# Optimization experiments

Hardware: AMD Instinct MI355X
Metric: run time of the kernel (lower is better)

Reference implementation:

```python
import jax, jax.numpy as jnp
import numpy as np

NEG = jnp.float32(-1e9)


def setup_inputs() -> dict:
    key = jax.random.key(0)
    ks = jax.random.split(key, 8)
    B, S, D = 8, 2048, 1024
    scale = 1.0 / np.sqrt(D)
    return {
        "xQ": jax.random.normal(ks[0], (B, S, D), jnp.float32),
        "xK": jax.random.normal(ks[1], (B, S, D), jnp.float32),
        "xV": jax.random.normal(ks[2], (B, S, D), jnp.float32),
        "padding_mask": jax.random.randint(ks[3], (B, S), 0, 2, jnp.int32),
        "casual_mask": jnp.ones((B, S), jnp.int32),
        "W_q": jax.random.normal(ks[4], (D, D), jnp.float32) * scale,
        "b_q": jnp.zeros((D,), jnp.float32),
        "W_k": jax.random.normal(ks[5], (D, D), jnp.float32) * scale,
        "b_k": jnp.zeros((D,), jnp.float32),
        "W_v": jax.random.normal(ks[6], (D, D), jnp.float32) * scale,
        "b_v": jnp.zeros((D,), jnp.float32),
    }


def reference(xQ, xK, xV, padding_mask, casual_mask, W_q, b_q, W_k, b_k, W_v, b_v):
    # Linear projections (torch nn.Linear: x @ W.T + b)
    Q = jnp.einsum('bsd,ed->bse', xQ, W_q) + b_q
    K = jnp.einsum('bsd,ed->bse', xK, W_k) + b_k
    V = jnp.einsum('bsd,ed->bse', xV, W_v) + b_v

    # Raw logits (note: original code applies NO 1/sqrt(dk) scaling)
    QKT = jnp.einsum('bqd,bkd->bqk', Q, K)  # [B, Sq, Sk]

    # Additive padding mask: -1e9 on padded key positions
    pad = jnp.where(padding_mask[:, None, :] == 0, NEG, jnp.float32(0.0))
    # Additive causal mask: -1e9 above the diagonal
    Sq, Sk = QKT.shape[1], QKT.shape[2]
    caus = jnp.where(
        jnp.tril(jnp.ones((Sq, Sk), dtype=bool)), jnp.float32(0.0), NEG
    )[None, :, :]
    QKT = QKT + pad + caus

    S = jax.nn.softmax(QKT, axis=-1)
    return jnp.einsum('bqk,bkd->bqd', S, V)
```

## Files before the change

kernel.cpp:

```cpp
#include <hip/hip_runtime.h>

typedef __attribute__((ext_vector_type(4))) float f4;
typedef __attribute__((ext_vector_type(4))) float f32x4;
typedef _Float16 half8 __attribute__((ext_vector_type(8)));

#define DEVI static __device__ __forceinline__

DEVI void gload_lds16(const void* g, void* l) {
  __builtin_amdgcn_global_load_lds(
      (const __attribute__((address_space(1))) void*)g,
      (__attribute__((address_space(3))) void*)l, 16, 0, 0);
}

DEVI int xcd_swz(int id, int n) {
  int q = n >> 3, r = n & 7;
  int x = id & 7, c = id >> 3;
  return (x < r ? x * (q + 1) : r * (q + 1) + (x - r) * q) + c;
}

#define FENCED_BARRIER()                \
  __builtin_amdgcn_sched_barrier(0);    \
  __builtin_amdgcn_s_barrier();         \
  __builtin_amdgcn_sched_barrier(0);

#define SWZ(kgv, rowv) ((((kgv) ^ ((rowv) >> 1)) & 3) * 8)

__global__ __launch_bounds__(256) void cvt_plain(const float* __restrict__ X,
                                                 _Float16* __restrict__ H,
                                                 int n4) {
  int i = blockIdx.x * 256 + threadIdx.x;
  const int stride = gridDim.x * 256;
  typedef _Float16 half4v __attribute__((ext_vector_type(4)));
  for (; i < n4; i += stride) {
    f4 x = ((const f4*)X)[i];
    half4v h;
#pragma unroll
    for (int j = 0; j < 4; ++j) h[j] = (_Float16)x[j];
    ((half4v*)H)[i] = h;
  }
}

__global__ __launch_bounds__(256) void cvt_split(const float* __restrict__ X,
                                                 _Float16* __restrict__ H,
                                                 _Float16* __restrict__ L,
                                                 int n4) {
  int i = blockIdx.x * 256 + threadIdx.x;
  const int stride = gridDim.x * 256;
  typedef _Float16 half4v __attribute__((ext_vector_type(4)));
  for (; i < n4; i += stride) {
    f4 x = ((const f4*)X)[i];
    half4v h, l;
#pragma unroll
    for (int j = 0; j < 4; ++j) {
      h[j] = (_Float16)x[j];
      l[j] = (_Float16)(x[j] - (float)h[j]);
    }
    ((half4v*)H)[i] = h;
    ((half4v*)L)[i] = l;
  }
}

DEVI void acc_zero44(f32x4 (&acc)[4][4]) {
#pragma unroll
  for (int i = 0; i < 4; ++i)
#pragma unroll
    for (int j = 0; j < 4; ++j) acc[i][j] = (f32x4)0.0f;
}
DEVI void acc_zero42(f32x4 (&acc)[4][2]) {
#pragma unroll
  for (int i = 0; i < 4; ++i)
#pragma unroll
    for (int j = 0; j < 2; ++j) acc[i][j] = (f32x4)0.0f;
}

template <int WSPLIT, int OUTMODE>
__global__ __launch_bounds__(512, 4) void proj3(
    const _Float16* __restrict__ X, const _Float16* __restrict__ Wh,
    const _Float16* __restrict__ Wl, const float* __restrict__ bias,
    _Float16* __restrict__ OutHi, _Float16* __restrict__ OutLo,
    _Float16* __restrict__ VtOut) {
  extern __shared__ _Float16 lds[];
  constexpr int ACH = 128 * 32;
  constexpr int BCH = 128 * 32;
  constexpr int CHUNK = ACH + BCH * (1 + WSPLIT);
  const int id = xcd_swz(blockIdx.x, gridDim.x);
  const int m0 = (id >> 3) * 128, n0 = (id & 7) * 128;
  const _Float16* A0 = X + (size_t)m0 * 1024;
  const _Float16* B0 = Wh + (size_t)n0 * 1024;
  const _Float16* B1 = Wl + (size_t)n0 * 1024;
  const int tid = threadIdx.x;
  const int w = tid >> 6, lane = tid & 63;
  const int wm = w >> 2, wn = w & 3;
  const int r16 = lane & 15, kg = lane >> 4;
  f32x4 acc[4][2];
  acc_zero42(acc);

  auto STAGE = [&](int t, int buf) {
    _Float16* base = lds + buf * CHUNK;
    int row = tid >> 2, c = tid & 3;
    int cs = (c ^ (row >> 1)) & 3;
    size_t src = (size_t)row * 1024 + t * 32 + cs * 8;
    gload_lds16(A0 + src, base + tid * 8);
    gload_lds16(B0 + src, base + ACH + tid * 8);
    if (WSPLIT) gload_lds16(B1 + src, base + ACH + BCH + tid * 8);
  };
  auto COMPUTE = [&](int buf) {
    const _Float16* la = lds + buf * CHUNK;
    const _Float16* lb = la + ACH;
    half8 a[4], b0f[2], b1f[2];
#pragma unroll
    for (int mi = 0; mi < 4; ++mi) {
      int row = wm * 64 + mi * 16 + r16;
      a[mi] = *(const half8*)(la + row * 32 + SWZ(kg, row));
    }
#pragma unroll
    for (int ni = 0; ni < 2; ++ni) {
      int row = wn * 32 + ni * 16 + r16;
      int off = row * 32 + SWZ(kg, row);
      b0f[ni] = *(const half8*)(lb + off);
      if (WSPLIT) b1f[ni] = *(const half8*)(lb + BCH + off);
    }
    __builtin_amdgcn_s_setprio(1);
#pragma unroll
    for (int mi = 0; mi < 4; ++mi)
#pragma unroll
      for (int ni = 0; ni < 2; ++ni) {
        acc[mi][ni] = __builtin_amdgcn_mfma_f32_16x16x32_f16(
            a[mi], b0f[ni], acc[mi][ni], 0, 0, 0);
        if (WSPLIT)
          acc[mi][ni] = __builtin_amdgcn_mfma_f32_16x16x32_f16(
              a[mi], b1f[ni], acc[mi][ni], 0, 0, 0);
      }
    __builtin_amdgcn_s_setprio(0);
  };

  const int NS = 32;
  STAGE(0, 0);
  STAGE(1, 1);
  int tt = 0;
  for (; tt < NS - 1; ++tt) {
    if constexpr (WSPLIT)
      asm volatile("s_waitcnt vmcnt(3)" ::: "memory");
    else
      asm volatile("s_waitcnt vmcnt(2)" ::: "memory");
    FENCED_BARRIER();
    if (tt + 2 < NS) STAGE(tt + 2, (tt + 2) % 3);
    COMPUTE(tt % 3);
  }
  asm volatile("s_waitcnt vmcnt(0)" ::: "memory");
  FENCED_BARRIER();
  COMPUTE(tt % 3);

  float bcol[2];
#pragma unroll
  for (int ni = 0; ni < 2; ++ni) bcol[ni] = bias[n0 + wn * 32 + ni * 16 + r16];

  if (OUTMODE != 2) {
#pragma unroll
    for (int mi = 0; mi < 4; ++mi) {
      int row = m0 + wm * 64 + mi * 16 + kg * 4;
#pragma unroll
      for (int ni = 0; ni < 2; ++ni) {
        int col = n0 + wn * 32 + ni * 16 + r16;
#pragma unroll
        for (int j = 0; j < 4; ++j) {
          float v = acc[mi][ni][j] + bcol[ni];
          _Float16 h = (_Float16)v;
          OutHi[(size_t)(row + j) * 1024 + col] = h;
          if (OUTMODE == 0)
            OutLo[(size_t)(row + j) * 1024 + col] = (_Float16)(v - (float)h);
        }
      }
    }
  } else {
    __syncthreads();
    _Float16(*T)[128] = (_Float16(*)[128])lds;
#pragma unroll
    for (int mi = 0; mi < 4; ++mi) {
      int ml = wm * 64 + mi * 16 + kg * 4;
#pragma unroll
      for (int ni = 0; ni < 2; ++ni) {
        int nl = wn * 32 + ni * 16 + r16;
#pragma unroll
        for (int j = 0; j < 4; ++j)
          T[nl][ml + j] = (_Float16)(acc[mi][ni][j] + bcol[ni]);
      }
    }
    __syncthreads();
    const int b = m0 >> 11;
    const int s0 = m0 & 2047;
#pragma unroll
    for (int r = 0; r < 4; ++r) {
      int flat = tid + r * 512;
      int n = flat >> 4, c = flat & 15;
      half8 v = *(const half8*)&T[n][c * 8];
      *(half8*)(VtOut + (size_t)b * (1024 * 2048) + (size_t)(n0 + n) * 2048 +
                s0 + c * 8) = v;
    }
  }
}

template <int WSPLIT, int OUTMODE>
__global__ __launch_bounds__(512, 2) void proj_fused(
    const float* __restrict__ X, const _Float16* __restrict__ Wh,
    const _Float16* __restrict__ Wl, const float* __restrict__ bias,
    _Float16* __restrict__ OutHi, _Float16* __restrict__ OutLo,
    _Float16* __restrict__ VtOut) {
  extern __shared__ _Float16 lds[];
  constexpr int ACH = 256 * 32;
  constexpr int BCH = 128 * 32;
  constexpr int CHUNK = ACH + BCH * (1 + WSPLIT);
  const int id = xcd_swz(blockIdx.x, gridDim.x);
  const int m0 = (id >> 3) * 256, n0 = (id & 7) * 128;
  const float* A = X + (size_t)m0 * 1024;
  const _Float16* B0 = Wh + (size_t)n0 * 1024;
  const _Float16* B1 = Wl + (size_t)n0 * 1024;
  const int tid = threadIdx.x;
  const int w = tid >> 6, lane = tid & 63;
  const int wm = w >> 1, wn = w & 1;
  const int r16 = lane & 15, kg = lane >> 4;
  f32x4 acc[4][4];
  acc_zero44(acc);
  f4 ra[4];

  auto ALOAD = [&](int t) {
#pragma unroll
    for (int j = 0; j < 2; ++j) {
      int g = tid + j * 512;
      int row = g >> 2, c = g & 3;
      const float* src = A + (size_t)row * 1024 + t * 32 + c * 8;
      ra[2 * j] = *(const f4*)src;
      ra[2 * j + 1] = *(const f4*)(src + 4);
    }
  };
  auto AWRITE = [&](int buf) {
    _Float16* ab = lds + buf * CHUNK;
#pragma unroll
    for (int j = 0; j < 2; ++j) {
      int g = tid + j * 512;
      int row = g >> 2, c = g & 3;
      half8 h;
#pragma unroll
      for (int e = 0; e < 4; ++e) {
        h[e] = (_Float16)ra[2 * j][e];
        h[e + 4] = (_Float16)ra[2 * j + 1][e];
      }
      *(half8*)(ab + (size_t)row * 32 + SWZ(c, row)) = h;
    }
  };
  auto WLOAD = [&](int t, int buf) {
    _Float16* bb = lds + buf * CHUNK + ACH;
    int row = tid >> 2, c = tid & 3;
    int cs = (c ^ (row >> 1)) & 3;
    gload_lds16(B0 + (size_t)row * 1024 + t * 32 + cs * 8, bb + tid * 8);
    if (WSPLIT)
      gload_lds16(B1 + (size_t)row * 1024 + t * 32 + cs * 8,
                  bb + BCH + tid * 8);
  };
  auto COMPUTE = [&](int buf) {
    const _Float16* la = lds + buf * CHUNK;
    const _Float16* lb = la + ACH;
    half8 a[4], b0f[4], b1f[4];
#pragma unroll
    for (int mi = 0; mi < 4; ++mi) {
      int row = wm * 64 + mi * 16 + r16;
      a[mi] = *(const half8*)(la + row * 32 + SWZ(kg, row));
    }
#pragma unroll
    for (int ni = 0; ni < 4; ++ni) {
      int row = wn * 64 + ni * 16 + r16;
      int off = row * 32 + SWZ(kg, row);
      b0f[ni] = *(const half8*)(lb + off);
      if (WSPLIT) b1f[ni] = *(const half8*)(lb + BCH + off);
    }
    __builtin_amdgcn_s_setprio(1);
#pragma unroll
    for (int mi = 0; mi < 4; ++mi)
#pragma unroll
      for (int ni = 0; ni < 4; ++ni) {
        acc[mi][ni] = __builtin_amdgcn_mfma_f32_16x16x32_f16(
            a[mi], b0f[ni], acc[mi][ni], 0, 0, 0);
        if (WSPLIT)
          acc[mi][ni] = __builtin_amdgcn_mfma_f32_16x16x32_f16(
              a[mi], b1f[ni], acc[mi][ni], 0, 0, 0);
      }
    __builtin_amdgcn_s_setprio(0);
  };

  const int NS = 32;
  WLOAD(0, 0);
  ALOAD(0);
  asm volatile("s_waitcnt vmcnt(0)" ::: "memory");
  __builtin_amdgcn_sched_barrier(0);
  AWRITE(0);
  asm volatile("s_waitcnt lgkmcnt(0)" ::: "memory");
  FENCED_BARRIER();
  for (int t = 0; t < NS; ++t) {
    if (t + 1 < NS) {
      WLOAD(t + 1, (t + 1) & 1);
      ALOAD(t + 1);
    }
    COMPUTE(t & 1);
    if (t + 1 < NS) {
      asm volatile("s_waitcnt vmcnt(0)" ::: "memory");
      __builtin_amdgcn_sched_barrier(0);
      AWRITE((t + 1) & 1);
      asm volatile("s_waitcnt lgkmcnt(0)" ::: "memory");
      FENCED_BARRIER();
    }
  }

  float bcol[4];
#pragma unroll
  for (int ni = 0; ni < 4; ++ni) bcol[ni] = bias[n0 + wn * 64 + ni * 16 + r16];

  if (OUTMODE != 2) {
#pragma unroll
    for (int mi = 0; mi < 4; ++mi) {
      int row = m0 + wm * 64 + mi * 16 + kg * 4;
#pragma unroll
      for (int ni = 0; ni < 4; ++ni) {
        int col = n0 + wn * 64 + ni * 16 + r16;
#pragma unroll
        for (int j = 0; j < 4; ++j) {
          float v = acc[mi][ni][j] + bcol[ni];
          _Float16 h = (_Float16)v;
          OutHi[(size_t)(row + j) * 1024 + col] = h;
          if (OUTMODE == 0)
            OutLo[(size_t)(row + j) * 1024 + col] = (_Float16)(v - (float)h);
        }
      }
    }
  } else {
    __syncthreads();
    _Float16(*T)[256] = (_Float16(*)[256])lds;
#pragma unroll
    for (int mi = 0; mi < 4; ++mi) {
      int ml = wm * 64 + mi * 16 + kg * 4;
#pragma unroll
      for (int ni = 0; ni < 4; ++ni) {
        int nl = wn * 64 + ni * 16 + r16;
#pragma unroll
        for (int j = 0; j < 4; ++j)
          T[nl][ml + j] = (_Float16)(acc[mi][ni][j] + bcol[ni]);
      }
    }
    __syncthreads();
    const int b = m0 >> 11;
    const int s0 = m0 & 2047;
#pragma unroll
    for (int r = 0; r < 8; ++r) {
      int flat = tid + r * 512;
      int n = flat >> 5, c = flat & 31;
      half8 v = *(const half8*)&T[n][c * 8];
      *(half8*)(VtOut + (size_t)b * (1024 * 2048) + (size_t)(n0 + n) * 2048 +
                s0 + c * 8) = v;
    }
  }
}

__global__ __launch_bounds__(512, 4) void qk_eng(
    const _Float16* __restrict__ Qh, const _Float16* __restrict__ Ql,
    const _Float16* __restrict__ Kh, float* __restrict__ Lg, int bbase) {
  extern __shared__ _Float16 lds[];
  constexpr int CHUNK = 12288;
  const int id = xcd_swz(blockIdx.x, gridDim.x);
  const int y = id / 144;
  int t = id % 144;
  int g4 = 0, base = 0;
  while (t >= base + (g4 + 1) * 4) { base += (g4 + 1) * 4; ++g4; }
  const int rem = t - base;
  const int qt = g4 * 4 + rem / (g4 + 1);
  const int kt = rem % (g4 + 1);
  const int b = bbase + y;
  const size_t boff = (size_t)b * (2048 * 1024);
  const _Float16* A0 = Qh + boff + (size_t)(qt * 64) * 1024;
  const _Float16* A1 = Ql + boff + (size_t)(qt * 64) * 1024;
  const _Float16* B0 = Kh + boff + (size_t)(kt * 256) * 1024;
  const int tid = threadIdx.x;
  const int w = tid >> 6, lane = tid & 63;
  const int r16 = lane & 15, kg = lane >> 4;
  const int wn = w;
  f32x4 acc[4][2];
  acc_zero42(acc);

  auto STAGE = [&](int t_, int buf) {
    _Float16* base_ = lds + buf * CHUNK;
    {
      int g = tid & 255;
      int row = g >> 2, c = g & 3;
      int cs = (c ^ (row >> 1)) & 3;
      const _Float16* src = (tid < 256) ? A0 : A1;
      _Float16* dst = base_ + ((tid < 256) ? 0 : 2048);
      gload_lds16(src + (size_t)row * 1024 + t_ * 32 + cs * 8, dst + g * 8);
    }
#pragma unroll
    for (int j = 0; j < 2; ++j) {
      int g = tid + j * 512;
      int row = g >> 2, c = g & 3;
      int cs = (c ^ (row >> 1)) & 3;
      gload_lds16(B0 + (size_t)row * 1024 + t_ * 32 + cs * 8,
                  base_ + 4096 + g * 8);
    }
  };
  auto COMPUTE = [&](int buf) {
    const _Float16* la = lds + buf * CHUNK;
    half8 a0[4], a1[4], bf[2];
#pragma unroll
    for (int mi = 0; mi < 4; ++mi) {
      int row = mi * 16 + r16;
      int off = row * 32 + SWZ(kg, row);
      a0[mi] = *(const half8*)(la + off);
      a1[mi] = *(const half8*)(la + 2048 + off);
    }
#pragma unroll
    for (int ni = 0; ni < 2; ++ni) {
      int row = wn * 32 + ni * 16 + r16;
      bf[ni] = *(const half8*)(la + 4096 + row * 32 + SWZ(kg, row));
    }
    __builtin_amdgcn_s_setprio(1);
#pragma unroll
    for (int mi = 0; mi < 4; ++mi)
#pragma unroll
      for (int ni = 0; ni < 2; ++ni) {
        acc[mi][ni] = __builtin_amdgcn_mfma_f32_16x16x32_f16(
            a0[mi], bf[ni], acc[mi][ni], 0, 0, 0);
        acc[mi][ni] = __builtin_amdgcn_mfma_f32_16x16x32_f16(
            a1[mi], bf[ni], acc[mi][ni], 0, 0, 0);
      }
    __builtin_amdgcn_s_setprio(0);
  };

  const int NS = 32;
  STAGE(0, 0);
  STAGE(1, 1);
  int tt = 0;
  for (; tt < NS - 1; ++tt) {
    asm volatile("s_waitcnt vmcnt(3)" ::: "memory");
    FENCED_BARRIER();
    if (tt + 2 < NS) STAGE(tt + 2, (tt + 2) % 3);
    COMPUTE(tt % 3);
  }
  asm volatile("s_waitcnt vmcnt(0)" ::: "memory");
  FENCED_BARRIER();
  COMPUTE(tt % 3);

  float* L = Lg + (size_t)y * (2048 * 2048);
#pragma unroll
  for (int mi = 0; mi < 4; ++mi) {
    int row = qt * 64 + mi * 16 + kg * 4;
#pragma unroll
    for (int ni = 0; ni < 2; ++ni) {
      int col = kt * 256 + wn * 32 + ni * 16 + r16;
#pragma unroll
      for (int j = 0; j < 4; ++j)
        L[(size_t)(row + j) * 2048 + col] = acc[mi][ni][j];
    }
  }
}

__global__ __launch_bounds__(512, 4) void pv_eng(
    const float* __restrict__ Lg, const _Float16* __restrict__ Vt,
    float* __restrict__ Out, int bbase) {
  extern __shared__ _Float16 lds[];
  constexpr int CHUNK = 8192;
  const int id = xcd_swz(blockIdx.x, gridDim.x);
  const int y = id >> 7;
  const int qt = (id & 127) >> 3, nt = id & 7;
  const int b = bbase + y;
  const _Float16* P = (const _Float16*)(Lg + (size_t)y * (2048 * 2048));
  const _Float16* A0 = P + (size_t)(qt * 128) * 4096;
  const _Float16* B0 =
      Vt + (size_t)b * (1024 * 2048) + (size_t)(nt * 128) * 2048;
  const int NS = (qt + 1) * 4;
  const int tid = threadIdx.x;
  const int w = tid >> 6, lane = tid & 63;
  const int wm = w >> 2, wn = w & 3;
  const int r16 = lane & 15, kg = lane >> 4;
  f32x4 acc[4][2];
  acc_zero42(acc);

  auto STAGE = [&](int t_, int buf) {
    _Float16* base_ = lds + buf * CHUNK;
    {
      int row = tid >> 2, c = tid & 3;
      int cs = (c ^ (row >> 1)) & 3;
      gload_lds16(A0 + (size_t)row * 4096 + t_ * 32 + cs * 8, base_ + tid * 8);
      gload_lds16(B0 + (size_t)row * 2048 + t_ * 32 + cs * 8,
                  base_ + 4096 + tid * 8);
    }
  };
  auto COMPUTE = [&](int buf) {
    const _Float16* la = lds + buf * CHUNK;
    half8 a[4], bf[2];
#pragma unroll
    for (int mi = 0; mi < 4; ++mi) {
      int row = wm * 64 + mi * 16 + r16;
      a[mi] = *(const half8*)(la + row * 32 + SWZ(kg, row));
    }
#pragma unroll
    for (int ni = 0; ni < 2; ++ni) {
      int row = wn * 32 + ni * 16 + r16;
      bf[ni] = *(const half8*)(la + 4096 + row * 32 + SWZ(kg, row));
    }
    __builtin_amdgcn_s_setprio(1);
#pragma unroll
    for (int mi = 0; mi < 4; ++mi)
#pragma unroll
      for (int ni = 0; ni < 2; ++ni)
        acc[mi][ni] = __builtin_amdgcn_mfma_f32_16x16x32_f16(
            a[mi], bf[ni], acc[mi][ni], 0, 0, 0);
    __builtin_amdgcn_s_setprio(0);
  };

  STAGE(0, 0);
  STAGE(1, 1);
  int tt = 0;
  for (; tt < NS - 1; ++tt) {
    asm volatile("s_waitcnt vmcnt(2)" ::: "memory");
    FENCED_BARRIER();
    if (tt + 2 < NS) STAGE(tt + 2, (tt + 2) % 3);
    COMPUTE(tt % 3);
  }
  asm volatile("s_waitcnt vmcnt(0)" ::: "memory");
  FENCED_BARRIER();
  COMPUTE(tt % 3);

#pragma unroll
  for (int mi = 0; mi < 4; ++mi) {
    int row = qt * 128 + wm * 64 + mi * 16 + kg * 4;
#pragma unroll
    for (int ni = 0; ni < 2; ++ni) {
      int col = nt * 128 + wn * 32 + ni * 16 + r16;
#pragma unroll
      for (int j = 0; j < 4; ++j)
        Out[(size_t)(b * 2048 + row + j) * 1024 + col] = acc[mi][ni][j];
    }
  }
}

__global__ __launch_bounds__(256) void softmax_kernel(
    float* __restrict__ Lg, const int* __restrict__ pad, int bbase) {
  const int q = blockIdx.x;
  const int y = blockIdx.y;
  const int b = bbase + y;
  const int tid = threadIdx.x;
  float* row = Lg + (size_t)y * (2048 * 2048) + (size_t)q * 2048;
  _Float16* prow = (_Float16*)row;
  const int* pb = pad + (size_t)b * 2048;
  const int kend = ((q >> 8) + 1) << 8;
  float v[8];
  int nv = 0;
  float mx = -3.0e38f;
  for (int k = tid; k <= q; k += 256) {
    float l = row[k];
    if (pb[k] == 0) l += -1.0e9f;
    v[nv++] = l;
    mx = fmaxf(mx, l);
  }
  __shared__ float red[4];
  for (int o = 32; o; o >>= 1) mx = fmaxf(mx, __shfl_xor(mx, o));
  if ((tid & 63) == 0) red[tid >> 6] = mx;
  __syncthreads();
  mx = fmaxf(fmaxf(red[0], red[1]), fmaxf(red[2], red[3]));
  __syncthreads();
  float s = 0.f;
  for (int i = 0; i < nv; ++i) s += expf(v[i] - mx);
  for (int o = 32; o; o >>= 1) s += __shfl_xor(s, o);
  if ((tid & 63) == 0) red[tid >> 6] = s;
  __syncthreads();
  s = red[0] + red[1] + red[2] + red[3];
  const float inv = 1.0f / s;
  int i = 0;
  for (int k = tid; k <= q; k += 256) {
    prow[k] = (_Float16)(expf(v[i] - mx) * inv);
    ++i;
  }
  for (int k = q + 1 + tid; k < kend; k += 256) prow[k] = (_Float16)0.0f;
}

__global__ __launch_bounds__(512) void fix_f(const int* __restrict__ pad,
                                             int* __restrict__ fb) {
  const int b = threadIdx.x >> 6, k = threadIdx.x & 63;
  unsigned long long m = __ballot(pad[b * 2048 + k] != 0);
  if (k == 0) fb[b] = m ? (__ffsll((long long)m) - 1) : 64;
}

__global__ __launch_bounds__(256) void fix_qrow2(
    const float* __restrict__ xQ, const float* __restrict__ Wq,
    const float* __restrict__ bq, const int* __restrict__ fb,
    float* __restrict__ Qrow) {
  const int b = blockIdx.y;
  const int f = fb[b];
  const int tid = threadIdx.x;
  const int e = blockIdx.x * 16 + (tid >> 4);
  const int l16 = tid & 15;
  __shared__ float xq[1024];
  for (int q = 0; q < f; ++q) {
    *(f4*)&xq[tid * 4] = ((const f4*)(xQ + (size_t)(b * 2048 + q) * 1024))[tid];
    __syncthreads();
    float a = 0.f;
#pragma unroll
    for (int it = 0; it < 16; ++it) {
      int d = l16 * 4 + it * 64;
      f4 ww = *(const f4*)(Wq + (size_t)e * 1024 + d);
      a += xq[d] * ww[0] + xq[d + 1] * ww[1] + xq[d + 2] * ww[2] +
           xq[d + 3] * ww[3];
    }
    for (int o = 8; o; o >>= 1) a += __shfl_xor(a, o);
    if (l16 == 0) Qrow[((size_t)b * 64 + q) * 1024 + e] = a + bq[e];
    __syncthreads();
  }
}

__global__ __launch_bounds__(256) void fix_qb0(const float* __restrict__ bk,
                                               const int* __restrict__ fb,
                                               const float* __restrict__ Qrow,
                                               float* __restrict__ qb0) {
  const int q = blockIdx.x, b = blockIdx.y;
  if (q >= fb[b]) return;
  const int tid = threadIdx.x;
  const float* qr = Qrow + ((size_t)b * 64 + q) * 1024;
  float p = 0.f;
  for (int e = tid; e < 1024; e += 256) p += qr[e] * bk[e];
  __shared__ float red[4];
  for (int o = 32; o; o >>= 1) p += __shfl_xor(p, o);
  if ((tid & 63) == 0) red[tid >> 6] = p;
  __syncthreads();
  if (tid == 0) qb0[b * 64 + q] = red[0] + red[1] + red[2] + red[3];
}

__global__ __launch_bounds__(256) void fix_g2(const float* __restrict__ Wk,
                                              const int* __restrict__ fb,
                                              const float* __restrict__ Qrow,
                                              float* __restrict__ Gpart) {
  const int b = blockIdx.y;
  const int f = fb[b];
  const int tid = threadIdx.x;
  const int ddblk = blockIdx.x & 3, es = blockIdx.x >> 2;
  const int dd = ddblk * 256 + tid;
  __shared__ float qc[128];
  for (int q = 0; q < f; ++q) {
    if (tid < 32)
      *(f4*)&qc[tid * 4] =
          ((const f4*)(Qrow + ((size_t)b * 64 + q) * 1024 + es * 128))[tid];
    __syncthreads();
    float g = 0.f;
    for (int e = 0; e < 128; ++e)
      g += qc[e] * Wk[(size_t)(es * 128 + e) * 1024 + dd];
    Gpart[(((size_t)es * 8 + b) * 64 + q) * 1024 + dd] = g;
    __syncthreads();
  }
}

__global__ __launch_bounds__(256) void fix_logit2(
    const float* __restrict__ xK, const int* __restrict__ pad,
    const int* __restrict__ fb, const float* __restrict__ Gpart,
    const float* __restrict__ qb0, float* __restrict__ lrow) {
  const int b = blockIdx.y;
  const int f = fb[b];
  const int tid = threadIdx.x;
  const int k = blockIdx.x * 16 + (tid >> 4);
  const int l16 = tid & 15;
  __shared__ float Gs[1024];
  for (int q = 0; q < f; ++q) {
    f4 s = (f4)0.0f;
#pragma unroll
    for (int es = 0; es < 8; ++es)
      s += ((const f4*)(Gpart + (((size_t)es * 8 + b) * 64 + q) * 1024))[tid];
    *(f4*)&Gs[tid * 4] = s;
    __syncthreads();
    float a = 0.f;
#pragma unroll
    for (int it = 0; it < 16; ++it) {
      int d = l16 * 4 + it * 64;
      f4 x = *(const f4*)(xK + (size_t)(b * 2048 + k) * 1024 + d);
      a += x[0] * Gs[d] + x[1] * Gs[d + 1] + x[2] * Gs[d + 2] +
           x[3] * Gs[d + 3];
    }
    for (int o = 8; o; o >>= 1) a += __shfl_xor(a, o);
    if (l16 == 0) {
      float l = a + qb0[b * 64 + q];
      if (pad[b * 2048 + k] == 0) l += -1.0e9f;
      if (k > q) l += -1.0e9f;
      lrow[((size_t)b * 64 + q) * 2048 + k] = l;
    }
    __syncthreads();
  }
}

__global__ __launch_bounds__(256) void fix_sm(const int* __restrict__ fb,
                                              float* __restrict__ lrow,
                                              float* __restrict__ srow) {
  const int q = blockIdx.x, b = blockIdx.y;
  if (q >= fb[b]) return;
  const int tid = threadIdx.x;
  float* row = lrow + ((size_t)b * 64 + q) * 2048;
  float v[8];
  float mx = -3.0e38f;
#pragma unroll
  for (int i = 0; i < 8; ++i) {
    v[i] = row[tid + i * 256];
    mx = fmaxf(mx, v[i]);
  }
  __shared__ float red[4];
  for (int o = 32; o; o >>= 1) mx = fmaxf(mx, __shfl_xor(mx, o));
  if ((tid & 63) == 0) red[tid >> 6] = mx;
  __syncthreads();
  mx = fmaxf(fmaxf(red[0], red[1]), fmaxf(red[2], red[3]));
  __syncthreads();
  float s = 0.f;
#pragma unroll
  for (int i = 0; i < 8; ++i) {
    v[i] = expf(v[i] - mx);
    s += v[i];
  }
#pragma unroll
  for (int i = 0; i < 8; ++i) row[tid + i * 256] = v[i];
  for (int o = 32; o; o >>= 1) s += __shfl_xor(s, o);
  if ((tid & 63) == 0) red[tid >> 6] = s;
  __syncthreads();
  if (tid == 0) srow[b * 64 + q] = red[0] + red[1] + red[2] + red[3];
}

__global__ __launch_bounds__(256) void fix_pv2(
    const _Float16* __restrict__ Vt, const int* __restrict__ fb,
    const float* __restrict__ lrow, const float* __restrict__ srow,
    float* __restrict__ Out) {
  const int b = blockIdx.y;
  const int f = fb[b];
  const int tid = threadIdx.x;
  const int d = blockIdx.x * 16 + (tid >> 4);
  const int l16 = tid & 15;
  __shared__ float ps[2048];
  for (int q = 0; q < f; ++q) {
    const f4* src = (const f4*)(lrow + ((size_t)b * 64 + q) * 2048);
    *(f4*)&ps[tid * 8] = src[tid * 2];
    *(f4*)&ps[tid * 8 + 4] = src[tid * 2 + 1];
    __syncthreads();
    float o = 0.f;
#pragma unroll
    for (int it = 0; it < 16; ++it) {
      int k = l16 * 8 + it * 128;
      half8 vv = *(const half8*)(Vt + (size_t)b * (1024 * 2048) +
                                 (size_t)d * 2048 + k);
      o += (float)vv[0] * ps[k] + (float)vv[1] * ps[k + 1] +
           (float)vv[2] * ps[k + 2] + (float)vv[3] * ps[k + 3] +
           (float)vv[4] * ps[k + 4] + (float)vv[5] * ps[k + 5] +
           (float)vv[6] * ps[k + 6] + (float)vv[7] * ps[k + 7];
    }
    for (int of = 8; of; of >>= 1) o += __shfl_xor(o, of);
    if (l16 == 0)
      Out[(size_t)(b * 2048 + q) * 1024 + d] = o * (1.0f / srow[b * 64 + q]);
    __syncthreads();
  }
}

extern "C" void kernel_launch(void* const* d_in, const int* in_sizes, int n_in,
                              void* d_out, int out_size, void* d_ws,
                              size_t ws_size, hipStream_t stream) {
  const float* xQ = (const float*)d_in[0];
  const float* xK = (const float*)d_in[1];
  const float* xV = (const float*)d_in[2];
  const int* pad = (const int*)d_in[3];
  const float* Wq = (const float*)d_in[5];
  const float* bq = (const float*)d_in[6];
  const float* Wk = (const float*)d_in[7];
  const float* bk = (const float*)d_in[8];
  const float* Wv = (const float*)d_in[9];
  const float* bv = (const float*)d_in[10];
  float* Out = (float*)d_out;

  const size_t MB = (size_t)1 << 20;
  char* wsb = (char*)d_ws;
  _Float16* Qh = (_Float16*)(wsb);
  _Float16* Ql = (_Float16*)(wsb + 32 * MB);
  _Float16* Kh = (_Float16*)(wsb + 64 * MB);
  _Float16* Vt = (_Float16*)(wsb + 96 * MB);
  float* Lg = (float*)(wsb + 128 * MB);

  size_t avail = (ws_size > 128 * MB) ? ws_size - 128 * MB : 0;
  int G = (int)(avail / (16 * MB));
  if (G > 8) G = 8;
  if (G < 1) G = 1;

  const int SM_P1 = 73728;
  const int SM_P0 = 49152;
  const int SM_F = 65536;
  const int SM_QK = 73728;
  const int SM_PV = 49152;
  (void)hipFuncSetAttribute((const void*)&proj3<1, 0>,
                            hipFuncAttributeMaxDynamicSharedMemorySize, SM_P1);
  (void)hipFuncSetAttribute((const void*)&proj3<1, 1>,
                            hipFuncAttributeMaxDynamicSharedMemorySize, SM_P1);
  (void)hipFuncSetAttribute((const void*)&proj3<0, 2>,
                            hipFuncAttributeMaxDynamicSharedMemorySize, SM_P0);
  (void)hipFuncSetAttribute((const void*)&proj_fused<1, 0>,
                            hipFuncAttributeMaxDynamicSharedMemorySize, SM_F);
  (void)hipFuncSetAttribute((const void*)&proj_fused<1, 1>,
                            hipFuncAttributeMaxDynamicSharedMemorySize, SM_F);
  (void)hipFuncSetAttribute((const void*)&proj_fused<0, 2>,
                            hipFuncAttributeMaxDynamicSharedMemorySize, SM_F);
  (void)hipFuncSetAttribute((const void*)&qk_eng,
                            hipFuncAttributeMaxDynamicSharedMemorySize, SM_QK);
  (void)hipFuncSetAttribute((const void*)&pv_eng,
                            hipFuncAttributeMaxDynamicSharedMemorySize, SM_PV);

  dim3 blk(256), eblk(512);

  if (ws_size >= 165 * MB) {
    {
      _Float16* sX = (_Float16*)(wsb);
      _Float16* sW = (_Float16*)(wsb + 32 * MB);
      cvt_plain<<<dim3(2048), blk, 0, stream>>>(xV, sX, 4194304);
      cvt_plain<<<dim3(1024), blk, 0, stream>>>(Wv, sW, 262144);
      proj3<0, 2><<<dim3(1024), eblk, SM_P0, stream>>>(sX, sW, sW, bv, nullptr,
                                                       nullptr, Vt);
    }
    {
      _Float16* sX = (_Float16*)(wsb);
      _Float16* sWh = (_Float16*)(wsb + 32 * MB);
      _Float16* sWl = (_Float16*)(wsb + 34 * MB);
      cvt_plain<<<dim3(2048), blk, 0, stream>>>(xK, sX, 4194304);
      cvt_split<<<dim3(1024), blk, 0, stream>>>(Wk, sWh, sWl, 262144);
      proj3<1, 1><<<dim3(1024), eblk, SM_P1, stream>>>(sX, sWh, sWl, bk, Kh,
                                                       nullptr, nullptr);
    }
    {
      _Float16* sX = (_Float16*)(wsb + 128 * MB);
      _Float16* sWh = (_Float16*)(wsb + 160 * MB);
      _Float16* sWl = (_Float16*)(wsb + 162 * MB);
      cvt_plain<<<dim3(2048), blk, 0, stream>>>(xQ, sX, 4194304);
      cvt_split<<<dim3(1024), blk, 0, stream>>>(Wq, sWh, sWl, 262144);
      proj3<1, 0><<<dim3(1024), eblk, SM_P1, stream>>>(sX, sWh, sWl, bq, Qh,
                                                       Ql, nullptr);
    }
  } else {
    _Float16* Wqh = (_Float16*)(wsb + 128 * MB);
    _Float16* Wql = (_Float16*)(wsb + 130 * MB);
    _Float16* Wkh = (_Float16*)(wsb + 132 * MB);
    _Float16* Wkl = (_Float16*)(wsb + 134 * MB);
    _Float16* Wvh = (_Float16*)(wsb + 136 * MB);
    cvt_split<<<dim3(1024), blk, 0, stream>>>(Wq, Wqh, Wql, 262144);
    cvt_split<<<dim3(1024), blk, 0, stream>>>(Wk, Wkh, Wkl, 262144);
    cvt_plain<<<dim3(1024), blk, 0, stream>>>(Wv, Wvh, 262144);
    proj_fused<0, 2><<<dim3(512), eblk, SM_F, stream>>>(xV, Wvh, Wvh, bv,
                                                        nullptr, nullptr, Vt);
    proj_fused<1, 1><<<dim3(512), eblk, SM_F, stream>>>(xK, Wkh, Wkl, bk, Kh,
                                                        nullptr, nullptr);
    proj_fused<1, 0><<<dim3(512), eblk, SM_F, stream>>>(xQ, Wqh, Wql, bq, Qh,
                                                        Ql, nullptr);
  }

  for (int bbase = 0; bbase < 8; bbase += G) {
    int nb = (8 - bbase < G) ? (8 - bbase) : G;
    qk_eng<<<dim3(144 * nb), eblk, SM_QK, stream>>>(Qh, Ql, Kh, Lg, bbase);
    softmax_kernel<<<dim3(2048, nb), blk, 0, stream>>>(Lg, pad, bbase);
    pv_eng<<<dim3(128 * nb), eblk, SM_PV, stream>>>(Lg, Vt, Out, bbase);
  }

  int* fb = (int*)(wsb);
  float* qb0 = (float*)(wsb + 4 * 1024);
  float* srow = (float*)(wsb + 8 * 1024);
  float* Qrow = (float*)(wsb + 1 * MB);
  float* Gpart = (float*)(wsb + 4 * MB);
  float* lrow = (float*)(wsb + 20 * MB);

  fix_f<<<dim3(1), dim3(512), 0, stream>>>(pad, fb);
  fix_qrow2<<<dim3(64, 8), blk, 0, stream>>>(xQ, Wq, bq, fb, Qrow);
  fix_qb0<<<dim3(64, 8), blk, 0, stream>>>(bk, fb, Qrow, qb0);
  fix_g2<<<dim3(32, 8), blk, 0, stream>>>(Wk, fb, Qrow, Gpart);
  fix_logit2<<<dim3(128, 8), blk, 0, stream>>>(xK, pad, fb, Gpart, qb0, lrow);
  fix_sm<<<dim3(64, 8), blk, 0, stream>>>(fb, lrow, srow);
  fix_pv2<<<dim3(64, 8), blk, 0, stream>>>(Vt, fb, lrow, srow, Out);
}
```

Baseline: 496.5 us.

## Retile QK to finer causal tiles, fold padding mask into QK epilogue, pair PV tiles

New measurement: 501.2 us. No clear change (+0.9%).

```diff
diff --git a/kernel.cpp b/kernel.cpp
--- a/kernel.cpp
+++ b/kernel.cpp
@@ -359,24 +359,23 @@
   }
 }
 
-__global__ __launch_bounds__(512, 4) void qk_eng(
+__global__ __launch_bounds__(256, 3) void qk_eng(
     const _Float16* __restrict__ Qh, const _Float16* __restrict__ Ql,
-    const _Float16* __restrict__ Kh, float* __restrict__ Lg, int bbase) {
+    const _Float16* __restrict__ Kh, const int* __restrict__ pad,
+    float* __restrict__ Lg, int bbase) {
   extern __shared__ _Float16 lds[];
-  constexpr int CHUNK = 12288;
+  constexpr int CHUNK = 8192;
   const int id = xcd_swz(blockIdx.x, gridDim.x);
-  const int y = id / 144;
-  int t = id % 144;
-  int g4 = 0, base = 0;
-  while (t >= base + (g4 + 1) * 4) { base += (g4 + 1) * 4; ++g4; }
-  const int rem = t - base;
-  const int qt = g4 * 4 + rem / (g4 + 1);
-  const int kt = rem % (g4 + 1);
+  const int y = id / 272;
+  int t = id % 272;
+  int qt = 0, base = 0;
+  while (t >= base + (qt >> 1) + 1) { base += (qt >> 1) + 1; ++qt; }
+  const int kt = t - base;
   const int b = bbase + y;
   const size_t boff = (size_t)b * (2048 * 1024);
   const _Float16* A0 = Qh + boff + (size_t)(qt * 64) * 1024;
   const _Float16* A1 = Ql + boff + (size_t)(qt * 64) * 1024;
-  const _Float16* B0 = Kh + boff + (size_t)(kt * 256) * 1024;
+  const _Float16* B0 = Kh + boff + (size_t)(kt * 128) * 1024;
   const int tid = threadIdx.x;
   const int w = tid >> 6, lane = tid & 63;
   const int r16 = lane & 15, kg = lane >> 4;
@@ -387,16 +386,15 @@
   auto STAGE = [&](int t_, int buf) {
     _Float16* base_ = lds + buf * CHUNK;
     {
-      int g = tid & 255;
-      int row = g >> 2, c = g & 3;
+      int row = tid >> 2, c = tid & 3;
       int cs = (c ^ (row >> 1)) & 3;
-      const _Float16* src = (tid < 256) ? A0 : A1;
-      _Float16* dst = base_ + ((tid < 256) ? 0 : 2048);
-      gload_lds16(src + (size_t)row * 1024 + t_ * 32 + cs * 8, dst + g * 8);
+      size_t src = (size_t)row * 1024 + t_ * 32 + cs * 8;
+      gload_lds16(A0 + src, base_ + tid * 8);
+      gload_lds16(A1 + src, base_ + 2048 + tid * 8);
     }
 #pragma unroll
     for (int j = 0; j < 2; ++j) {
-      int g = tid + j * 512;
+      int g = tid + j * 256;
       int row = g >> 2, c = g & 3;
       int cs = (c ^ (row >> 1)) & 3;
       gload_lds16(B0 + (size_t)row * 1024 + t_ * 32 + cs * 8,
@@ -436,7 +434,7 @@
   STAGE(1, 1);
   int tt = 0;
   for (; tt < NS - 1; ++tt) {
-    asm volatile("s_waitcnt vmcnt(3)" ::: "memory");
+    asm volatile("s_waitcnt vmcnt(4)" ::: "memory");
     FENCED_BARRIER();
     if (tt + 2 < NS) STAGE(tt + 2, (tt + 2) % 3);
     COMPUTE(tt % 3);
@@ -446,115 +444,120 @@
   COMPUTE(tt % 3);
 
   float* L = Lg + (size_t)y * (2048 * 2048);
-#pragma unroll
-  for (int mi = 0; mi < 4; ++mi) {
-    int row = qt * 64 + mi * 16 + kg * 4;
-#pragma unroll
-    for (int ni = 0; ni < 2; ++ni) {
-      int col = kt * 256 + wn * 32 + ni * 16 + r16;
+  const int* pb = pad + (size_t)b * 2048;
+#pragma unroll
+  for (int ni = 0; ni < 2; ++ni) {
+    int col = kt * 128 + wn * 32 + ni * 16 + r16;
+    const float padd = (pb[col] == 0) ? -1.0e9f : 0.0f;
+#pragma unroll
+    for (int mi = 0; mi < 4; ++mi) {
+      int row = qt * 64 + mi * 16 + kg * 4;
 #pragma unroll
       for (int j = 0; j < 4; ++j)
-        L[(size_t)(row + j) * 2048 + col] = acc[mi][ni][j];
+        L[(size_t)(row + j) * 2048 + col] = acc[mi][ni][j] + padd;
     }
   }
 }
 
 __global__ __launch_bounds__(512, 4) void pv_eng(
     const float* __restrict__ Lg, const _Float16* __restrict__ Vt,
-    float* __restrict__ Out, int bbase) {
+    float* __restrict__ Out, int bbase, int ntiles) {
   extern __shared__ _Float16 lds[];
   constexpr int CHUNK = 8192;
-  const int id = xcd_swz(blockIdx.x, gridDim.x);
-  const int y = id >> 7;
-  const int qt = (id & 127) >> 3, nt = id & 7;
-  const int b = bbase + y;
-  const _Float16* P = (const _Float16*)(Lg + (size_t)y * (2048 * 2048));
-  const _Float16* A0 = P + (size_t)(qt * 128) * 4096;
-  const _Float16* B0 =
-      Vt + (size_t)b * (1024 * 2048) + (size_t)(nt * 128) * 2048;
-  const int NS = (qt + 1) * 4;
+  const int g0 = xcd_swz(blockIdx.x, gridDim.x);
   const int tid = threadIdx.x;
   const int w = tid >> 6, lane = tid & 63;
   const int wm = w >> 2, wn = w & 3;
   const int r16 = lane & 15, kg = lane >> 4;
-  f32x4 acc[4][2];
-  acc_zero42(acc);
-
-  auto STAGE = [&](int t_, int buf) {
-    _Float16* base_ = lds + buf * CHUNK;
-    {
+
+  for (int half = 0; half < 2; ++half) {
+    const int idt = half ? (ntiles - 1 - g0) : g0;
+    const int y = idt >> 7;
+    const int qt = (idt & 127) >> 3, nt = idt & 7;
+    const int b = bbase + y;
+    const _Float16* P = (const _Float16*)(Lg + (size_t)y * (2048 * 2048));
+    const _Float16* A0 = P + (size_t)(qt * 128) * 4096;
+    const _Float16* B0 =
+        Vt + (size_t)b * (1024 * 2048) + (size_t)(nt * 128) * 2048;
+    const int NS = (qt + 1) * 4;
+    f32x4 acc[4][2];
+    acc_zero42(acc);
+
+    auto STAGE = [&](int t_, int buf) {
+      _Float16* base_ = lds + buf * CHUNK;
       int row = tid >> 2, c = tid & 3;
       int cs = (c ^ (row >> 1)) & 3;
       gload_lds16(A0 + (size_t)row * 4096 + t_ * 32 + cs * 8, base_ + tid * 8);
       gload_lds16(B0 + (size_t)row * 2048 + t_ * 32 + cs * 8,
                   base_ + 4096 + tid * 8);
-    }
-  };
-  auto COMPUTE = [&](int buf) {
-    const _Float16* la = lds + buf * CHUNK;
-    half8 a[4], bf[2];
+    };
+    auto COMPUTE = [&](int buf) {
+      const _Float16* la = lds + buf * CHUNK;
+      half8 a[4], bf[2];
+#pragma unroll
+      for (int mi = 0; mi < 4; ++mi) {
+        int row = wm * 64 + mi * 16 + r16;
+        a[mi] = *(const half8*)(la + row * 32 + SWZ(kg, row));
+      }
+#pragma unroll
+      for (int ni = 0; ni < 2; ++ni) {
+        int row = wn * 32 + ni * 16 + r16;
+        bf[ni] = *(const half8*)(la + 4096 + row * 32 + SWZ(kg, row));
+      }
+      __builtin_amdgcn_s_setprio(1);
+#pragma unroll
+      for (int mi = 0; mi < 4; ++mi)
+#pragma unroll
+        for (int ni = 0; ni < 2; ++ni)
+          acc[mi][ni] = __builtin_amdgcn_mfma_f32_16x16x32_f16(
+              a[mi], bf[ni], acc[mi][ni], 0, 0, 0);
+      __builtin_amdgcn_s_setprio(0);
+    };
+
+    STAGE(0, 0);
+    STAGE(1, 1);
+    int tt = 0;
+    for (; tt < NS - 1; ++tt) {
+      asm volatile("s_waitcnt vmcnt(2)" ::: "memory");
+      FENCED_BARRIER();
+      if (tt + 2 < NS) STAGE(tt + 2, (tt + 2) % 3);
+      COMPUTE(tt % 3);
+    }
+    asm volatile("s_waitcnt vmcnt(0)" ::: "memory");
+    FENCED_BARRIER();
+    COMPUTE(tt % 3);
+
 #pragma unroll
     for (int mi = 0; mi < 4; ++mi) {
-      int row = wm * 64 + mi * 16 + r16;
-      a[mi] = *(const half8*)(la + row * 32 + SWZ(kg, row));
-    }
-#pragma unroll
-    for (int ni = 0; ni < 2; ++ni) {
-      int row = wn * 32 + ni * 16 + r16;
-      bf[ni] = *(const half8*)(la + 4096 + row * 32 + SWZ(kg, row));
-    }
-    __builtin_amdgcn_s_setprio(1);
-#pragma unroll
-    for (int mi = 0; mi < 4; ++mi)
-#pragma unroll
-      for (int ni = 0; ni < 2; ++ni)
-        acc[mi][ni] = __builtin_amdgcn_mfma_f32_16x16x32_f16(
-            a[mi], bf[ni], acc[mi][ni], 0, 0, 0);
-    __builtin_amdgcn_s_setprio(0);
-  };
-
-  STAGE(0, 0);
-  STAGE(1, 1);
-  int tt = 0;
-  for (; tt < NS - 1; ++tt) {
-    asm volatile("s_waitcnt vmcnt(2)" ::: "memory");
-    FENCED_BARRIER();
-    if (tt + 2 < NS) STAGE(tt + 2, (tt + 2) % 3);
-    COMPUTE(tt % 3);
-  }
-  asm volatile("s_waitcnt vmcnt(0)" ::: "memory");
-  FENCED_BARRIER();
-  COMPUTE(tt % 3);
-
-#pragma unroll
-  for (int mi = 0; mi < 4; ++mi) {
-    int row = qt * 128 + wm * 64 + mi * 16 + kg * 4;
-#pragma unroll
-    for (int ni = 0; ni < 2; ++ni) {
-      int col = nt * 128 + wn * 32 + ni * 16 + r16;
-#pragma unroll
-      for (int j = 0; j < 4; ++j)
-        Out[(size_t)(b * 2048 + row + j) * 1024 + col] = acc[mi][ni][j];
-    }
-  }
-}
-
-__global__ __launch_bounds__(256) void softmax_kernel(
-    float* __restrict__ Lg, const int* __restrict__ pad, int bbase) {
+      int row = qt * 128 + wm * 64 + mi * 16 + kg * 4;
+#pragma unroll
+      for (int ni = 0; ni < 2; ++ni) {
+        int col = nt * 128 + wn * 32 + ni * 16 + r16;
+#pragma unroll
+        for (int j = 0; j < 4; ++j)
+          Out[(size_t)(b * 2048 + row + j) * 1024 + col] = acc[mi][ni][j];
+      }
+    }
+    if (half == 0) {
+      asm volatile("s_waitcnt vmcnt(0) lgkmcnt(0)" ::: "memory");
+      FENCED_BARRIER();
+    }
+  }
+}
+
+__global__ __launch_bounds__(256) void softmax_kernel(float* __restrict__ Lg,
+                                                      int bbase) {
   const int q = blockIdx.x;
   const int y = blockIdx.y;
-  const int b = bbase + y;
   const int tid = threadIdx.x;
   float* row = Lg + (size_t)y * (2048 * 2048) + (size_t)q * 2048;
   _Float16* prow = (_Float16*)row;
-  const int* pb = pad + (size_t)b * 2048;
   const int kend = ((q >> 8) + 1) << 8;
   float v[8];
   int nv = 0;
   float mx = -3.0e38f;
   for (int k = tid; k <= q; k += 256) {
     float l = row[k];
-    if (pb[k] == 0) l += -1.0e9f;
     v[nv++] = l;
     mx = fmaxf(mx, l);
   }
@@ -787,7 +790,7 @@
   const int SM_P1 = 73728;
   const int SM_P0 = 49152;
   const int SM_F = 65536;
-  const int SM_QK = 73728;
+  const int SM_QK = 49152;
   const int SM_PV = 49152;
   (void)hipFuncSetAttribute((const void*)&proj3<1, 0>,
                             hipFuncAttributeMaxDynamicSharedMemorySize, SM_P1);
@@ -854,9 +857,10 @@
 
   for (int bbase = 0; bbase < 8; bbase += G) {
     int nb = (8 - bbase < G) ? (8 - bbase) : G;
-    qk_eng<<<dim3(144 * nb), eblk, SM_QK, stream>>>(Qh, Ql, Kh, Lg, bbase);
-    softmax_kernel<<<dim3(2048, nb), blk, 0, stream>>>(Lg, pad, bbase);
-    pv_eng<<<dim3(128 * nb), eblk, SM_PV, stream>>>(Lg, Vt, Out, bbase);
+    qk_eng<<<dim3(272 * nb), blk, SM_QK, stream>>>(Qh, Ql, Kh, pad, Lg, bbase);
+    softmax_kernel<<<dim3(2048, nb), blk, 0, stream>>>(Lg, bbase);
+    pv_eng<<<dim3(64 * nb), eblk, SM_PV, stream>>>(Lg, Vt, Out, bbase,
+                                                   128 * nb);
   }
 
   int* fb = (int*)(wsb);
```

## Fold padding mask into QK epilogue and pair PV tiles for load balance

Applied to the files above, without the earlier changes.

Measured after the change: 496.1 us. Within noise of the previous version (-0.1%).

```diff
diff --git a/kernel.cpp b/kernel.cpp
--- a/kernel.cpp
+++ b/kernel.cpp
@@ -361,7 +361,8 @@
 
 __global__ __launch_bounds__(512, 4) void qk_eng(
     const _Float16* __restrict__ Qh, const _Float16* __restrict__ Ql,
-    const _Float16* __restrict__ Kh, float* __restrict__ Lg, int bbase) {
+    const _Float16* __restrict__ Kh, const int* __restrict__ pad,
+    float* __restrict__ Lg, int bbase) {
   extern __shared__ _Float16 lds[];
   constexpr int CHUNK = 12288;
   const int id = xcd_swz(blockIdx.x, gridDim.x);
@@ -446,115 +447,120 @@
   COMPUTE(tt % 3);
 
   float* L = Lg + (size_t)y * (2048 * 2048);
-#pragma unroll
-  for (int mi = 0; mi < 4; ++mi) {
-    int row = qt * 64 + mi * 16 + kg * 4;
-#pragma unroll
-    for (int ni = 0; ni < 2; ++ni) {
-      int col = kt * 256 + wn * 32 + ni * 16 + r16;
+  const int* pb = pad + (size_t)b * 2048;
+#pragma unroll
+  for (int ni = 0; ni < 2; ++ni) {
+    int col = kt * 256 + wn * 32 + ni * 16 + r16;
+    const float padd = (pb[col] == 0) ? -1.0e9f : 0.0f;
+#pragma unroll
+    for (int mi = 0; mi < 4; ++mi) {
+      int row = qt * 64 + mi * 16 + kg * 4;
 #pragma unroll
       for (int j = 0; j < 4; ++j)
-        L[(size_t)(row + j) * 2048 + col] = acc[mi][ni][j];
+        L[(size_t)(row + j) * 2048 + col] = acc[mi][ni][j] + padd;
     }
   }
 }
 
 __global__ __launch_bounds__(512, 4) void pv_eng(
     const float* __restrict__ Lg, const _Float16* __restrict__ Vt,
-    float* __restrict__ Out, int bbase) {
+    float* __restrict__ Out, int bbase, int ntiles) {
   extern __shared__ _Float16 lds[];
   constexpr int CHUNK = 8192;
-  const int id = xcd_swz(blockIdx.x, gridDim.x);
-  const int y = id >> 7;
-  const int qt = (id & 127) >> 3, nt = id & 7;
-  const int b = bbase + y;
-  const _Float16* P = (const _Float16*)(Lg + (size_t)y * (2048 * 2048));
-  const _Float16* A0 = P + (size_t)(qt * 128) * 4096;
-  const _Float16* B0 =
-      Vt + (size_t)b * (1024 * 2048) + (size_t)(nt * 128) * 2048;
-  const int NS = (qt + 1) * 4;
+  const int g0 = xcd_swz(blockIdx.x, gridDim.x);
   const int tid = threadIdx.x;
   const int w = tid >> 6, lane = tid & 63;
   const int wm = w >> 2, wn = w & 3;
   const int r16 = lane & 15, kg = lane >> 4;
-  f32x4 acc[4][2];
-  acc_zero42(acc);
-
-  auto STAGE = [&](int t_, int buf) {
-    _Float16* base_ = lds + buf * CHUNK;
-    {
+
+  for (int half = 0; half < 2; ++half) {
+    const int idt = half ? (ntiles - 1 - g0) : g0;
+    const int y = idt >> 7;
+    const int qt = (idt & 127) >> 3, nt = idt & 7;
+    const int b = bbase + y;
+    const _Float16* P = (const _Float16*)(Lg + (size_t)y * (2048 * 2048));
+    const _Float16* A0 = P + (size_t)(qt * 128) * 4096;
+    const _Float16* B0 =
+        Vt + (size_t)b * (1024 * 2048) + (size_t)(nt * 128) * 2048;
+    const int NS = (qt + 1) * 4;
+    f32x4 acc[4][2];
+    acc_zero42(acc);
+
+    auto STAGE = [&](int t_, int buf) {
+      _Float16* base_ = lds + buf * CHUNK;
       int row = tid >> 2, c = tid & 3;
       int cs = (c ^ (row >> 1)) & 3;
       gload_lds16(A0 + (size_t)row * 4096 + t_ * 32 + cs * 8, base_ + tid * 8);
       gload_lds16(B0 + (size_t)row * 2048 + t_ * 32 + cs * 8,
                   base_ + 4096 + tid * 8);
-    }
-  };
-  auto COMPUTE = [&](int buf) {
-    const _Float16* la = lds + buf * CHUNK;
-    half8 a[4], bf[2];
+    };
+    auto COMPUTE = [&](int buf) {
+      const _Float16* la = lds + buf * CHUNK;
+      half8 a[4], bf[2];
+#pragma unroll
+      for (int mi = 0; mi < 4; ++mi) {
+        int row = wm * 64 + mi * 16 + r16;
+        a[mi] = *(const half8*)(la + row * 32 + SWZ(kg, row));
+      }
+#pragma unroll
+      for (int ni = 0; ni < 2; ++ni) {
+        int row = wn * 32 + ni * 16 + r16;
+        bf[ni] = *(const half8*)(la + 4096 + row * 32 + SWZ(kg, row));
+      }
+      __builtin_amdgcn_s_setprio(1);
+#pragma unroll
+      for (int mi = 0; mi < 4; ++mi)
+#pragma unroll
+        for (int ni = 0; ni < 2; ++ni)
+          acc[mi][ni] = __builtin_amdgcn_mfma_f32_16x16x32_f16(
+              a[mi], bf[ni], acc[mi][ni], 0, 0, 0);
+      __builtin_amdgcn_s_setprio(0);
+    };
+
+    STAGE(0, 0);
+    STAGE(1, 1);
+    int tt = 0;
+    for (; tt < NS - 1; ++tt) {
+      asm volatile("s_waitcnt vmcnt(2)" ::: "memory");
+      FENCED_BARRIER();
+      if (tt + 2 < NS) STAGE(tt + 2, (tt + 2) % 3);
+      COMPUTE(tt % 3);
+    }
+    asm volatile("s_waitcnt vmcnt(0)" ::: "memory");
+    FENCED_BARRIER();
+    COMPUTE(tt % 3);
+
 #pragma unroll
     for (int mi = 0; mi < 4; ++mi) {
-      int row = wm * 64 + mi * 16 + r16;
-      a[mi] = *(const half8*)(la + row * 32 + SWZ(kg, row));
-    }
-#pragma unroll
-    for (int ni = 0; ni < 2; ++ni) {
-      int row = wn * 32 + ni * 16 + r16;
-      bf[ni] = *(const half8*)(la + 4096 + row * 32 + SWZ(kg, row));
-    }
-    __builtin_amdgcn_s_setprio(1);
-#pragma unroll
-    for (int mi = 0; mi < 4; ++mi)
-#pragma unroll
-      for (int ni = 0; ni < 2; ++ni)
-        acc[mi][ni] = __builtin_amdgcn_mfma_f32_16x16x32_f16(
-            a[mi], bf[ni], acc[mi][ni], 0, 0, 0);
-    __builtin_amdgcn_s_setprio(0);
-  };
-
-  STAGE(0, 0);
-  STAGE(1, 1);
-  int tt = 0;
-  for (; tt < NS - 1; ++tt) {
-    asm volatile("s_waitcnt vmcnt(2)" ::: "memory");
-    FENCED_BARRIER();
-    if (tt + 2 < NS) STAGE(tt + 2, (tt + 2) % 3);
-    COMPUTE(tt % 3);
-  }
-  asm volatile("s_waitcnt vmcnt(0)" ::: "memory");
-  FENCED_BARRIER();
-  COMPUTE(tt % 3);
-
-#pragma unroll
-  for (int mi = 0; mi < 4; ++mi) {
-    int row = qt * 128 + wm * 64 + mi * 16 + kg * 4;
-#pragma unroll
-    for (int ni = 0; ni < 2; ++ni) {
-      int col = nt * 128 + wn * 32 + ni * 16 + r16;
-#pragma unroll
-      for (int j = 0; j < 4; ++j)
-        Out[(size_t)(b * 2048 + row + j) * 1024 + col] = acc[mi][ni][j];
-    }
-  }
-}
-
-__global__ __launch_bounds__(256) void softmax_kernel(
-    float* __restrict__ Lg, const int* __restrict__ pad, int bbase) {
+      int row = qt * 128 + wm * 64 + mi * 16 + kg * 4;
+#pragma unroll
+      for (int ni = 0; ni < 2; ++ni) {
+        int col = nt * 128 + wn * 32 + ni * 16 + r16;
+#pragma unroll
+        for (int j = 0; j < 4; ++j)
+          Out[(size_t)(b * 2048 + row + j) * 1024 + col] = acc[mi][ni][j];
+      }
+    }
+    if (half == 0) {
+      asm volatile("s_waitcnt vmcnt(0) lgkmcnt(0)" ::: "memory");
+      FENCED_BARRIER();
+    }
+  }
+}
+
+__global__ __launch_bounds__(256) void softmax_kernel(float* __restrict__ Lg,
+                                                      int bbase) {
   const int q = blockIdx.x;
   const int y = blockIdx.y;
-  const int b = bbase + y;
   const int tid = threadIdx.x;
   float* row = Lg + (size_t)y * (2048 * 2048) + (size_t)q * 2048;
   _Float16* prow = (_Float16*)row;
-  const int* pb = pad + (size_t)b * 2048;
   const int kend = ((q >> 8) + 1) << 8;
   float v[8];
   int nv = 0;
   float mx = -3.0e38f;
   for (int k = tid; k <= q; k += 256) {
     float l = row[k];
-    if (pb[k] == 0) l += -1.0e9f;
     v[nv++] = l;
     mx = fmaxf(mx, l);
   }
@@ -854,9 +860,11 @@
 
   for (int bbase = 0; bbase < 8; bbase += G) {
     int nb = (8 - bbase < G) ? (8 - bbase) : G;
-    qk_eng<<<dim3(144 * nb), eblk, SM_QK, stream>>>(Qh, Ql, Kh, Lg, bbase);
-    softmax_kernel<<<dim3(2048, nb), blk, 0, stream>>>(Lg, pad, bbase);
-    pv_eng<<<dim3(128 * nb), eblk, SM_PV, stream>>>(Lg, Vt, Out, bbase);
+    qk_eng<<<dim3(144 * nb), eblk, SM_QK, stream>>>(Qh, Ql, Kh, pad, Lg,
+                                                    bbase);
+    softmax_kernel<<<dim3(2048, nb), blk, 0, stream>>>(Lg, bbase);
+    pv_eng<<<dim3(64 * nb), eblk, SM_PV, stream>>>(Lg, Vt, Out, bbase,
+                                                   128 * nb);
   }
 
   int* fb = (int*)(wsb);
```
